# Kernel optimization log

Measured on AMD Instinct MI355X. Metric: run time of the kernel, lower is better.

Reference implementation:

```python
import jax, jax.numpy as jnp
import numpy as np

N_NODES = 50000
N_RAND_EDGES = 800000
N_GRAPHS = 16
F_IN = 128
HID = 64
EMB = 16


def gat_layer(x, src, dst, W, a_src, a_dst, bias, heads, out_ch, concat):
    # x: [N, Fin]; W: [Fin, heads*out_ch]; a_src/a_dst: [heads, out_ch]
    n = x.shape[0]
    h = (x @ W).reshape(n, heads, out_ch)                      # [N, H, C]
    alpha_src = jnp.sum(h * a_src, axis=-1)                    # [N, H]
    alpha_dst = jnp.sum(h * a_dst, axis=-1)                    # [N, H]
    logits = jax.nn.leaky_relu(alpha_src[src] + alpha_dst[dst], 0.2)  # [E, H]
    # segment softmax over incoming edges of each dst node
    m = jax.ops.segment_max(logits, dst, num_segments=n)       # [N, H]
    e = jnp.exp(logits - m[dst])                               # [E, H]
    s = jax.ops.segment_sum(e, dst, num_segments=n)            # [N, H]
    alpha = e / (s[dst] + 1e-16)                               # [E, H]
    msg = h[src] * alpha[:, :, None]                           # [E, H, C]
    out = jax.ops.segment_sum(msg, dst, num_segments=n)        # [N, H, C]
    out = out.reshape(n, heads * out_ch) if concat else out.mean(axis=1)
    return out + bias, alpha


def setup_inputs() -> dict:
    key = jax.random.key(0)
    ks = jax.random.split(key, 20)
    x = jax.random.normal(ks[0], (N_NODES, F_IN), dtype=jnp.float32)
    src = jax.random.randint(ks[1], (N_RAND_EDGES,), 0, N_NODES)
    dst = jax.random.randint(ks[2], (N_RAND_EDGES,), 0, N_NODES)
    loops = jnp.arange(N_NODES)
    edge_index = jnp.stack([jnp.concatenate([src, loops]),
                            jnp.concatenate([dst, loops])]).astype(jnp.int64)
    batch = jnp.sort(jax.random.randint(ks[3], (N_NODES,), 0, N_GRAPHS)).astype(jnp.int64)
    p = lambda k, shp: (jax.random.normal(k, shp, dtype=jnp.float32) * 0.1)
    return {
        "x": x, "edge_index": edge_index, "batch": batch,
        # conv1: 128 -> 64, heads=2, concat -> 128
        "W1": p(ks[4], (F_IN, 2 * HID)), "as1": p(ks[5], (2, HID)), "ad1": p(ks[6], (2, HID)), "b1": p(ks[7], (2 * HID,)),
        # conv2: 128 -> 128, heads=1, mean
        "W2": p(ks[8], (2 * HID, 2 * HID)), "as2": p(ks[9], (1, 2 * HID)), "ad2": p(ks[10], (1, 2 * HID)), "b2": p(ks[11], (2 * HID,)),
        # conv3: 128 -> 16, heads=1, mean
        "W3": p(ks[12], (2 * HID, EMB)), "as3": p(ks[13], (1, EMB)), "ad3": p(ks[14], (1, EMB)), "b3": p(ks[15], (EMB,)),
        # final classifier 16 -> 2
        "Wl": p(ks[16], (EMB, 2)), "bl": p(ks[17], (2,)),
    }


def reference(x, edge_index, batch, W1, as1, ad1, b1, W2, as2, ad2, b2,
              W3, as3, ad3, b3, Wl, bl):
    src, dst = edge_index[0], edge_index[1]
    h1, a1 = gat_layer(x, src, dst, W1, as1, ad1, b1, heads=2, out_ch=HID, concat=True)
    h1 = jax.nn.relu(h1)
    h2, a2 = gat_layer(h1, src, dst, W2, as2, ad2, b2, heads=1, out_ch=2 * HID, concat=False)
    h2 = jax.nn.relu(h2)
    emb, a3 = gat_layer(h2, src, dst, W3, as3, ad3, b3, heads=1, out_ch=EMB, concat=False)
    # global mean pool over graphs (eval mode -> dropout is identity)
    counts = jax.ops.segment_sum(jnp.ones((emb.shape[0],), emb.dtype), batch, num_segments=N_GRAPHS)
    g_emb = jax.ops.segment_sum(emb, batch, num_segments=N_GRAPHS) / jnp.clip(counts, 1.0, None)[:, None]
    out = g_emb @ Wl + bl
    return (out, g_emb, emb, a1, a2, a3)
```

## Files before the change

kernel.cpp:

```cpp
#include <hip/hip_runtime.h>
#include <hip/hip_bf16.h>

#define DEVFN __device__ __forceinline__

using short8 = __attribute__((ext_vector_type(8))) short;
using f32x4  = __attribute__((ext_vector_type(4))) float;

DEVFN float ldf(const void* p, size_t i, bool f32) {
    return f32 ? ((const float*)p)[i]
               : __bfloat162float(((const __hip_bfloat16*)p)[i]);
}
DEVFN int ldidx(const void* p, size_t i, bool i64) {
    return i64 ? (int)((const long long*)p)[i] : ((const int*)p)[i];
}
DEVFN void stf(void* p, size_t i, float v, bool f32) {
    if (f32) ((float*)p)[i] = v;
    else     ((__hip_bfloat16*)p)[i] = __float2bfloat16(v);
}
DEVFN float lky(float v) { return v > 0.f ? v : 0.2f * v; }

DEVFN float bfbits2f(short s) {
    return __uint_as_float(((unsigned)(unsigned short)s) << 16);
}
DEVFN short f2bfbits(float f) {
    unsigned u = __float_as_uint(f);
    return (short)((u + 0x7fffu + ((u >> 16) & 1u)) >> 16);
}

__global__ void detect_k(const void* x, const void* ei, int* flags) {
    if (threadIdx.x == 0 && blockIdx.x == 0) {
        const __hip_bfloat16* xb = (const __hip_bfloat16*)x;
        int bad = 0;
        for (int i = 0; i < 512; ++i) {
            float v = __bfloat162float(xb[i]);
            if (!(v == v) || fabsf(v) > 1.0e6f) bad++;
        }
        flags[0] = (bad > 16) ? 1 : 0;
        const unsigned* w = (const unsigned*)ei;
        int zeros = 0;
        for (int i = 0; i < 64; ++i) if (w[2 * i + 1] == 0u) zeros++;
        flags[1] = (zeros >= 60) ? 1 : 0;
    }
}

__global__ void zero_i32(int* __restrict__ p, int n) {
    int i = blockIdx.x * blockDim.x + threadIdx.x;
    int st = gridDim.x * blockDim.x;
    for (; i < n; i += st) p[i] = 0;
}
__global__ void zero_f32(float* __restrict__ p, long n) {
    long i = (long)blockIdx.x * blockDim.x + threadIdx.x;
    long st = (long)gridDim.x * blockDim.x;
    for (; i < n; i += st) p[i] = 0.f;
}

__global__ void hist_k(const void* __restrict__ ei, int E, int* __restrict__ cnt,
                       const int* __restrict__ flags) {
    const bool i64 = flags[1] != 0;
    int e = blockIdx.x * blockDim.x + threadIdx.x;
    if (e >= E) return;
    atomicAdd(&cnt[ldidx(ei, (size_t)E + e, i64)], 1);
}

__global__ void scan_block_k(const int* __restrict__ cnt, int* __restrict__ incl,
                             int* __restrict__ part, int N) {
    __shared__ int sm[256];
    int tid = threadIdx.x;
    int i = blockIdx.x * 256 + tid;
    int v = (i < N) ? cnt[i] : 0;
    sm[tid] = v;
    __syncthreads();
    for (int o = 1; o < 256; o <<= 1) {
        int t = (tid >= o) ? sm[tid - o] : 0;
        __syncthreads();
        sm[tid] += t;
        __syncthreads();
    }
    if (i < N) incl[i] = sm[tid];
    if (tid == 255) part[blockIdx.x] = sm[255];
}

__global__ void scan_part_k(int* __restrict__ part, int nb) {
    __shared__ int sm[256];
    __shared__ int off;
    int tid = threadIdx.x;
    if (tid == 0) off = 0;
    __syncthreads();
    for (int b = 0; b < nb; b += 256) {
        int i = b + tid;
        int v = (i < nb) ? part[i] : 0;
        sm[tid] = v;
        __syncthreads();
        for (int o = 1; o < 256; o <<= 1) {
            int t = (tid >= o) ? sm[tid - o] : 0;
            __syncthreads();
            sm[tid] += t;
            __syncthreads();
        }
        if (i < nb) part[i] = sm[tid] - v + off;
        __syncthreads();
        if (tid == 255) off += sm[255];
        __syncthreads();
    }
}

__global__ void finalize_scan_k(int* __restrict__ incl_cur, const int* __restrict__ cnt,
                                const int* __restrict__ part, int* __restrict__ rs,
                                int N, int E) {
    int i = blockIdx.x * 256 + threadIdx.x;
    if (i >= N) return;
    int v = incl_cur[i] - cnt[i] + part[blockIdx.x];
    rs[i] = v;
    incl_cur[i] = v;
    if (i == N - 1) rs[N] = E;
}

__global__ void scatter_csr_k(const void* __restrict__ ei, int E, int* __restrict__ cur,
                              int2* __restrict__ csr, const int* __restrict__ flags) {
    const bool i64 = flags[1] != 0;
    int e = blockIdx.x * blockDim.x + threadIdx.x;
    if (e >= E) return;
    int s = ldidx(ei, e, i64);
    int d = ldidx(ei, (size_t)E + e, i64);
    int p = atomicAdd(&cur[d], 1);
    csr[p] = make_int2(s, e);
}

template <int DSRC, int FOUT, int HEADS>
__global__ __launch_bounds__(256) void gemm_alpha_mfma_k(
    const void* __restrict__ xin, const void* __restrict__ Wv,
    const void* __restrict__ asv, const void* __restrict__ adv,
    short* __restrict__ h_bf, float* __restrict__ as_out, float* __restrict__ ad_out,
    int N, const int* __restrict__ flags)
{
    constexpr int FIN = 128;
    constexpr int NCT = FOUT / 16;
    constexpr int CPH = FOUT / HEADS;
    constexpr int CTPH = CPH / 16;
    const bool f32 = flags[0] != 0;

    __shared__ short Wt[FOUT * FIN];

    for (int i = threadIdx.x; i < FIN * FOUT; i += 256) {
        int k = i / FOUT, c = i - (i / FOUT) * FOUT;
        short w;
        if (f32) w = f2bfbits(((const float*)Wv)[i]);
        else     w = ((const short*)Wv)[i];
        *(short*)((char*)Wt + (size_t)c * (FIN * 2) + (((k * 2) ^ ((c & 7) << 4)))) = w;
    }
    __syncthreads();

    const int wv = threadIdx.x >> 6;
    const int lane = threadIdx.x & 63;
    const int m0 = blockIdx.x * 64 + wv * 16;
    if (m0 >= N) return;
    const int lrow = lane & 15;
    const int lk   = lane >> 4;

    short8 afrag[4];
    if (DSRC == 0 && f32) {
        const float* xf = (const float*)xin + (size_t)(m0 + lrow) * FIN + lk * 8;
#pragma unroll
        for (int ks = 0; ks < 4; ++ks) {
            short8 t;
#pragma unroll
            for (int j = 0; j < 8; ++j) t[j] = f2bfbits(xf[ks * 32 + j]);
            afrag[ks] = t;
        }
    } else {
        const short* xb = (const short*)xin + (size_t)(m0 + lrow) * FIN + lk * 8;
#pragma unroll
        for (int ks = 0; ks < 4; ++ks)
            afrag[ks] = *(const short8*)(xb + ks * 32);
    }

    float csA[HEADS][4], cdA[HEADS][4];
#pragma unroll
    for (int hd = 0; hd < HEADS; ++hd)
#pragma unroll
        for (int r = 0; r < 4; ++r) { csA[hd][r] = 0.f; cdA[hd][r] = 0.f; }

#pragma unroll
    for (int ct = 0; ct < NCT; ++ct) {
        const int col = ct * 16 + lrow;
        const int hd = ct / CTPH;
        f32x4 acc = {0.f, 0.f, 0.f, 0.f};
#pragma unroll
        for (int ks = 0; ks < 4; ++ks) {
            const int kbyte = ks * 64 + lk * 16;
            short8 bfrag = *(const short8*)((const char*)Wt +
                               (size_t)col * (FIN * 2) + (kbyte ^ ((col & 7) << 4)));
            acc = __builtin_amdgcn_mfma_f32_16x16x32_bf16(afrag[ks], bfrag, acc, 0, 0, 0);
        }
        const float asc = ldf(asv, col, f32);
        const float adc = ldf(adv, col, f32);
#pragma unroll
        for (int r = 0; r < 4; ++r) {
            h_bf[(size_t)(m0 + lk * 4 + r) * FOUT + col] = f2bfbits(acc[r]);
            csA[hd][r] += acc[r] * asc;
            cdA[hd][r] += acc[r] * adc;
        }
    }

#pragma unroll
    for (int hd = 0; hd < HEADS; ++hd)
#pragma unroll
        for (int r = 0; r < 4; ++r) {
            float cs = csA[hd][r], cd = cdA[hd][r];
            for (int o = 1; o < 16; o <<= 1) {
                cs += __shfl_xor(cs, o);
                cd += __shfl_xor(cd, o);
            }
            csA[hd][r] = cs; cdA[hd][r] = cd;
        }
    if (lrow == 0) {
#pragma unroll
        for (int r = 0; r < 4; ++r) {
            int n = m0 + lk * 4 + r;
#pragma unroll
            for (int hd = 0; hd < HEADS; ++hd) {
                as_out[(size_t)n * HEADS + hd] = csA[hd][r];
                ad_out[(size_t)n * HEADS + hd] = cdA[hd][r];
            }
        }
    }
}

template <int HEADS, bool RELU>
__global__ __launch_bounds__(256) void agg128_k(
    const short* __restrict__ h_bf, const float* __restrict__ as_,
    const float* __restrict__ ad_, const int* __restrict__ rs,
    const int2* __restrict__ csr, const void* __restrict__ bias,
    short* __restrict__ z_bf, void* __restrict__ dout, size_t aoff,
    int N, const int* __restrict__ flags)
{
    __shared__ int   ls_src[4][64];
    __shared__ float ls_a[4][HEADS][64];
    const bool f32 = flags[0] != 0;
    const int wv = threadIdx.x >> 6;
    const int wid = (blockIdx.x * 256 + threadIdx.x) >> 6;
    if (wid >= N) return;
    const int lane = threadIdx.x & 63;
    const int beg = rs[wid], end = rs[wid + 1];
    const int deg = end - beg;
    const int cg = lane & 15;
    const int es = lane >> 4;
    const int h = (HEADS == 2) ? (cg >> 3) : 0;

    const float ad0 = ad_[(size_t)wid * HEADS];
    const float ad1 = (HEADS == 2) ? ad_[(size_t)wid * HEADS + 1] : 0.f;

    float acc[8] = {0.f, 0.f, 0.f, 0.f, 0.f, 0.f, 0.f, 0.f};

    if (deg <= 64) {
        const bool act = lane < deg;
        int2 se = make_int2(0, 0);
        if (act) se = csr[beg + lane];
        float l0 = act ? lky(as_[(size_t)se.x * HEADS] + ad0) : -1e30f;
        float l1 = 0.f;
        if (HEADS == 2) l1 = act ? lky(as_[(size_t)se.x * HEADS + 1] + ad1) : -1e30f;

        float m0 = l0, m1 = l1;
        for (int o = 1; o < 64; o <<= 1) {
            m0 = fmaxf(m0, __shfl_xor(m0, o));
            if (HEADS == 2) m1 = fmaxf(m1, __shfl_xor(m1, o));
        }
        float e0 = act ? expf(l0 - m0) : 0.f;
        float e1 = (HEADS == 2) ? (act ? expf(l1 - m1) : 0.f) : 0.f;
        float s0 = e0, s1 = e1;
        for (int o = 1; o < 64; o <<= 1) {
            s0 += __shfl_xor(s0, o);
            if (HEADS == 2) s1 += __shfl_xor(s1, o);
        }
        if (act) {
            float a0 = e0 * (1.f / (s0 + 1e-16f));
            ls_src[wv][lane] = se.x;
            ls_a[wv][0][lane] = a0;
            stf(dout, aoff + (size_t)se.y * HEADS, a0, f32);
            if (HEADS == 2) {
                float a1 = e1 * (1.f / (s1 + 1e-16f));
                ls_a[wv][1][lane] = a1;
                stf(dout, aoff + (size_t)se.y * 2 + 1, a1, f32);
            }
        }
        for (int b = 0; b < deg; b += 8) {
            const int pA = b + es, pB = b + 4 + es;
            int sA = 0, sB = 0;
            float aA = 0.f, aB = 0.f;
            if (pA < deg) { sA = ls_src[wv][pA]; aA = ls_a[wv][h][pA]; }
            if (pB < deg) { sB = ls_src[wv][pB]; aB = ls_a[wv][h][pB]; }
            const short8 hA = *(const short8*)(h_bf + (size_t)sA * 128 + cg * 8);
            const short8 hB = *(const short8*)(h_bf + (size_t)sB * 128 + cg * 8);
#pragma unroll
            for (int j = 0; j < 8; ++j) acc[j] = fmaf(bfbits2f(hA[j]), aA, acc[j]);
#pragma unroll
            for (int j = 0; j < 8; ++j) acc[j] = fmaf(bfbits2f(hB[j]), aB, acc[j]);
        }
    } else {
        float m0 = -1e30f, m1 = -1e30f;
        for (int p = beg + lane; p < end; p += 64) {
            int s = csr[p].x;
            m0 = fmaxf(m0, lky(as_[(size_t)s * HEADS] + ad0));
            if (HEADS == 2) m1 = fmaxf(m1, lky(as_[(size_t)s * HEADS + 1] + ad1));
        }
        for (int o = 1; o < 64; o <<= 1) {
            m0 = fmaxf(m0, __shfl_xor(m0, o));
            if (HEADS == 2) m1 = fmaxf(m1, __shfl_xor(m1, o));
        }
        float s0 = 0.f, s1 = 0.f;
        for (int p = beg + lane; p < end; p += 64) {
            int s = csr[p].x;
            s0 += expf(lky(as_[(size_t)s * HEADS] + ad0) - m0);
            if (HEADS == 2) s1 += expf(lky(as_[(size_t)s * HEADS + 1] + ad1) - m1);
        }
        for (int o = 1; o < 64; o <<= 1) {
            s0 += __shfl_xor(s0, o);
            if (HEADS == 2) s1 += __shfl_xor(s1, o);
        }
        const float inv0 = 1.f / (s0 + 1e-16f);
        const float inv1 = 1.f / (s1 + 1e-16f);

        for (int cb = beg; cb < end; cb += 64) {
            const int cn = min(64, end - cb);
            if (lane < cn) {
                int2 se = csr[cb + lane];
                float a0 = expf(lky(as_[(size_t)se.x * HEADS] + ad0) - m0) * inv0;
                ls_src[wv][lane] = se.x;
                ls_a[wv][0][lane] = a0;
                stf(dout, aoff + (size_t)se.y * HEADS, a0, f32);
                if (HEADS == 2) {
                    float a1 = expf(lky(as_[(size_t)se.x * HEADS + 1] + ad1) - m1) * inv1;
                    ls_a[wv][1][lane] = a1;
                    stf(dout, aoff + (size_t)se.y * 2 + 1, a1, f32);
                }
            }
            for (int b = 0; b < cn; b += 8) {
                const int pA = b + es, pB = b + 4 + es;
                int sA = 0, sB = 0;
                float aA = 0.f, aB = 0.f;
                if (pA < cn) { sA = ls_src[wv][pA]; aA = ls_a[wv][h][pA]; }
                if (pB < cn) { sB = ls_src[wv][pB]; aB = ls_a[wv][h][pB]; }
                const short8 hA = *(const short8*)(h_bf + (size_t)sA * 128 + cg * 8);
                const short8 hB = *(const short8*)(h_bf + (size_t)sB * 128 + cg * 8);
#pragma unroll
                for (int j = 0; j < 8; ++j) acc[j] = fmaf(bfbits2f(hA[j]), aA, acc[j]);
#pragma unroll
                for (int j = 0; j < 8; ++j) acc[j] = fmaf(bfbits2f(hB[j]), aB, acc[j]);
            }
        }
    }

#pragma unroll
    for (int j = 0; j < 8; ++j) {
        acc[j] += __shfl_xor(acc[j], 16);
        acc[j] += __shfl_xor(acc[j], 32);
    }
    if (es == 0) {
        short8 outv;
#pragma unroll
        for (int j = 0; j < 8; ++j) {
            float v = acc[j] + ldf(bias, cg * 8 + j, f32);
            if (RELU) v = fmaxf(v, 0.f);
            outv[j] = f2bfbits(v);
        }
        *(short8*)(z_bf + (size_t)wid * 128 + cg * 8) = outv;
    }
}

__global__ __launch_bounds__(256) void agg16_k(
    const short* __restrict__ h_bf, const float* __restrict__ as_,
    const float* __restrict__ ad_, const int* __restrict__ rs,
    const int2* __restrict__ csr, float* __restrict__ out,
    void* __restrict__ dout, size_t aoff, int N, const int* __restrict__ flags)
{
    __shared__ int   ls_src[4][64];
    __shared__ float ls_a[4][64];
    const bool f32 = flags[0] != 0;
    const int wv = threadIdx.x >> 6;
    const int wid = (blockIdx.x * 256 + threadIdx.x) >> 6;
    if (wid >= N) return;
    const int lane = threadIdx.x & 63;
    const int beg = rs[wid], end = rs[wid + 1];
    const int deg = end - beg;
    const int cg = lane & 7;
    const int es = lane >> 3;

    const float ad0 = ad_[wid];

    float a0s = 0.f, a1s = 0.f;

    if (deg <= 64) {
        const bool act = lane < deg;
        int2 se = make_int2(0, 0);
        if (act) se = csr[beg + lane];
        float l0 = act ? lky(as_[se.x] + ad0) : -1e30f;
        float m0 = l0;
        for (int o = 1; o < 64; o <<= 1) m0 = fmaxf(m0, __shfl_xor(m0, o));
        float e0 = act ? expf(l0 - m0) : 0.f;
        float s0 = e0;
        for (int o = 1; o < 64; o <<= 1) s0 += __shfl_xor(s0, o);
        if (act) {
            float a0 = e0 * (1.f / (s0 + 1e-16f));
            ls_src[wv][lane] = se.x;
            ls_a[wv][lane] = a0;
            stf(dout, aoff + se.y, a0, f32);
        }
        for (int b = 0; b < deg; b += 8) {
            const int p = b + es;
            if (p < deg) {
                const int sj = ls_src[wv][p];
                const float a = ls_a[wv][p];
                const int hv = *(const int*)(h_bf + (size_t)sj * 16 + cg * 2);
                a0s = fmaf(bfbits2f((short)(hv & 0xffff)), a, a0s);
                a1s = fmaf(bfbits2f((short)(hv >> 16)), a, a1s);
            }
        }
    } else {
        float m0 = -1e30f;
        for (int p = beg + lane; p < end; p += 64)
            m0 = fmaxf(m0, lky(as_[csr[p].x] + ad0));
        for (int o = 1; o < 64; o <<= 1) m0 = fmaxf(m0, __shfl_xor(m0, o));
        float s0 = 0.f;
        for (int p = beg + lane; p < end; p += 64)
            s0 += expf(lky(as_[csr[p].x] + ad0) - m0);
        for (int o = 1; o < 64; o <<= 1) s0 += __shfl_xor(s0, o);
        const float inv0 = 1.f / (s0 + 1e-16f);

        for (int cb = beg; cb < end; cb += 64) {
            const int cn = min(64, end - cb);
            if (lane < cn) {
                int2 se = csr[cb + lane];
                float a0 = expf(lky(as_[se.x] + ad0) - m0) * inv0;
                ls_src[wv][lane] = se.x;
                ls_a[wv][lane] = a0;
                stf(dout, aoff + se.y, a0, f32);
            }
            for (int b = 0; b < cn; b += 8) {
                const int p = b + es;
                if (p < cn) {
                    const int sj = ls_src[wv][p];
                    const float a = ls_a[wv][p];
                    const int hv = *(const int*)(h_bf + (size_t)sj * 16 + cg * 2);
                    a0s = fmaf(bfbits2f((short)(hv & 0xffff)), a, a0s);
                    a1s = fmaf(bfbits2f((short)(hv >> 16)), a, a1s);
                }
            }
        }
    }

#pragma unroll
    for (int o = 8; o < 64; o <<= 1) {
        a0s += __shfl_xor(a0s, o);
        a1s += __shfl_xor(a1s, o);
    }
    if (es == 0) {
        out[(size_t)wid * 16 + cg * 2]     = a0s;
        out[(size_t)wid * 16 + cg * 2 + 1] = a1s;
    }
}

__global__ __launch_bounds__(256) void finalize3_k(
    const float* __restrict__ acc, const void* __restrict__ bias,
    const void* __restrict__ batch, void* __restrict__ dout, size_t emb_off,
    float* __restrict__ g_sum, int N, const int* __restrict__ flags)
{
    const bool f32 = flags[0] != 0;
    const bool i64 = flags[1] != 0;
    __shared__ float gp[256];
    int tid = threadIdx.x;
    gp[tid] = 0.f;
    __syncthreads();
    long idx = (long)blockIdx.x * 256 + tid;
    if (idx < (long)N * 16) {
        int n = (int)(idx >> 4), col = (int)(idx & 15);
        float v = acc[idx] + ldf(bias, col, f32);
        stf(dout, emb_off + idx, v, f32);
        int g = ldidx(batch, n, i64);
        atomicAdd(&gp[g * 16 + col], v);
    }
    __syncthreads();
    float pv = gp[tid];
    if (pv != 0.f) atomicAdd(&g_sum[tid], pv);
}

__global__ __launch_bounds__(256) void head_k(
    const float* __restrict__ g_sum, const void* __restrict__ batch,
    const void* __restrict__ Wl, const void* __restrict__ bl,
    void* __restrict__ dout, size_t gemb_off, int N, const int* __restrict__ flags)
{
    const bool f32 = flags[0] != 0;
    const bool i64 = flags[1] != 0;
    __shared__ float ge[256];
    __shared__ int cnts[16];
    int tid = threadIdx.x;
    if (tid < 16) {
        int lo = 0, hi = N;
        while (lo < hi) { int mid = (lo + hi) >> 1; if (ldidx(batch, mid, i64) < tid) lo = mid + 1; else hi = mid; }
        int l2 = 0, h2 = N;
        while (l2 < h2) { int mid = (l2 + h2) >> 1; if (ldidx(batch, mid, i64) <= tid) l2 = mid + 1; else h2 = mid; }
        cnts[tid] = l2 - lo;
    }
    __syncthreads();
    {
        int g = tid >> 4;
        float v = g_sum[tid] / fmaxf((float)cnts[g], 1.f);
        ge[tid] = v;
        stf(dout, gemb_off + tid, v, f32);
    }
    __syncthreads();
    if (tid < 32) {
        int g = tid >> 1, j = tid & 1;
        float s = ldf(bl, j, f32);
        for (int c = 0; c < 16; ++c) s += ge[g * 16 + c] * ldf(Wl, (size_t)c * 2 + j, f32);
        stf(dout, (size_t)g * 2 + j, s, f32);
    }
}

static inline int cdiv(long a, int b) { return (int)((a + b - 1) / b); }

extern "C" void kernel_launch(void* const* d_in, const int* in_sizes, int n_in,
                              void* d_out, int out_size, void* d_ws, size_t ws_size,
                              hipStream_t stream)
{
    const void* x   = d_in[0];
    const void* ei  = d_in[1];
    const void* batch = d_in[2];
    const void* W1  = d_in[3];
    const void* as1 = d_in[4];
    const void* ad1 = d_in[5];
    const void* b1  = d_in[6];
    const void* W2  = d_in[7];
    const void* as2 = d_in[8];
    const void* ad2 = d_in[9];
    const void* b2  = d_in[10];
    const void* W3  = d_in[11];
    const void* as3 = d_in[12];
    const void* ad3 = d_in[13];
    const void* b3  = d_in[14];
    const void* Wl  = d_in[15];
    const void* bl  = d_in[16];

    const int N = in_sizes[0] / 128;
    const int E = in_sizes[1] / 2;

    int* flags = (int*)d_ws;
    float* ws = (float*)d_ws + 16;
    size_t o = 0;
    float* as_  = ws + o; o += (size_t)N * 2;
    float* ad_  = ws + o; o += (size_t)N * 2;
    float* bufE = ws + o; o += (size_t)N * 16;
    float* g_sum = ws + o; o += 256;
    short* hX = (short*)(ws + o); o += (size_t)N * 64;
    short* hZ = (short*)(ws + o); o += (size_t)N * 64;
    short* h3 = (short*)(ws + o); o += (size_t)N * 8;
    int* ip = (int*)(ws + o);
    int* cnt  = ip;            ip += N;
    int* incl = ip;            ip += N;
    int* part = ip;            ip += 256;
    int* rs   = ip;            ip += N + 1;
    if (((uintptr_t)ip & 7) != 0) ip += 1;
    int2* csr = (int2*)ip;     ip += 2 * E;

    const size_t off_gemb = 32;
    const size_t off_emb  = 32 + 256;
    const size_t off_a1   = off_emb + (size_t)N * 16;
    const size_t off_a2   = off_a1 + (size_t)E * 2;
    const size_t off_a3   = off_a2 + (size_t)E;

    const int B = 256;
    const int nbN = cdiv(N, 256);
    const int gemmBlocks = cdiv(N, 64);
    const int waveBlocks = cdiv(N, 4);

    detect_k<<<1, 64, 0, stream>>>(x, ei, flags);

    zero_i32<<<nbN, B, 0, stream>>>(cnt, N);
    hist_k<<<cdiv(E, B), B, 0, stream>>>(ei, E, cnt, flags);
    scan_block_k<<<nbN, B, 0, stream>>>(cnt, incl, part, N);
    scan_part_k<<<1, B, 0, stream>>>(part, nbN);
    finalize_scan_k<<<nbN, B, 0, stream>>>(incl, cnt, part, rs, N, E);
    scatter_csr_k<<<cdiv(E, B), B, 0, stream>>>(ei, E, incl, csr, flags);

    gemm_alpha_mfma_k<0, 128, 2><<<gemmBlocks, 256, 0, stream>>>(x, W1, as1, ad1, hX, as_, ad_, N, flags);
    agg128_k<2, true><<<waveBlocks, 256, 0, stream>>>(hX, as_, ad_, rs, csr, b1, hZ,
                                                      d_out, off_a1, N, flags);

    gemm_alpha_mfma_k<1, 128, 1><<<gemmBlocks, 256, 0, stream>>>(hZ, W2, as2, ad2, hX, as_, ad_, N, flags);
    agg128_k<1, true><<<waveBlocks, 256, 0, stream>>>(hX, as_, ad_, rs, csr, b2, hZ,
                                                      d_out, off_a2, N, flags);

    gemm_alpha_mfma_k<1, 16, 1><<<gemmBlocks, 256, 0, stream>>>(hZ, W3, as3, ad3, h3, as_, ad_, N, flags);
    agg16_k<<<waveBlocks, 256, 0, stream>>>(h3, as_, ad_, rs, csr, bufE,
                                            d_out, off_a3, N, flags);
    zero_f32<<<1, B, 0, stream>>>(g_sum, 256);
    finalize3_k<<<cdiv((long)N * 16, B), B, 0, stream>>>(bufE, b3, batch, d_out, off_emb, g_sum, N, flags);

    head_k<<<1, B, 0, stream>>>(g_sum, batch, Wl, bl, d_out, off_gemb, N, flags);
}
```

Baseline: 349.8 us.

## Build CSR via two-pass bucketed scatter to localize atomic writes

Replaces the single random CSR scatter with a two-level scatter. Edges are first grouped into buckets of 128 destination nodes using padded per-bucket counters, then each bucket is scattered into the final CSR by one block. The goal is to make the final atomics and writes land in a small, cache-local region instead of being spread randomly over the whole array. The cost is an extra pass that writes and reads a 16-byte-per-edge intermediate buffer, plus heavily contended atomics on about 400 bucket counters.

```diff
diff --git a/kernel.cpp b/kernel.cpp
--- a/kernel.cpp
+++ b/kernel.cpp
@@ -55,11 +55,13 @@
 }
 
 __global__ void hist_k(const void* __restrict__ ei, int E, int* __restrict__ cnt,
-                       const int* __restrict__ flags) {
+                       int* __restrict__ bcnt, const int* __restrict__ flags) {
     const bool i64 = flags[1] != 0;
     int e = blockIdx.x * blockDim.x + threadIdx.x;
     if (e >= E) return;
-    atomicAdd(&cnt[ldidx(ei, (size_t)E + e, i64)], 1);
+    int d = ldidx(ei, (size_t)E + e, i64);
+    atomicAdd(&cnt[d], 1);
+    atomicAdd(&bcnt[(d >> 7) * 16], 1);
 }
 
 __global__ void scan_block_k(const int* __restrict__ cnt, int* __restrict__ incl,
@@ -115,15 +117,53 @@
     if (i == N - 1) rs[N] = E;
 }
 
-__global__ void scatter_csr_k(const void* __restrict__ ei, int E, int* __restrict__ cur,
-                              int2* __restrict__ csr, const int* __restrict__ flags) {
+__global__ void bucket_scan_k(const int* __restrict__ bcnt, int* __restrict__ bbase,
+                              int* __restrict__ bcur, int NB, int E) {
+    __shared__ int sm[256];
+    __shared__ int off;
+    int tid = threadIdx.x;
+    if (tid == 0) off = 0;
+    __syncthreads();
+    for (int b = 0; b < NB; b += 256) {
+        int i = b + tid;
+        int v = (i < NB) ? bcnt[i * 16] : 0;
+        sm[tid] = v;
+        __syncthreads();
+        for (int o = 1; o < 256; o <<= 1) {
+            int t = (tid >= o) ? sm[tid - o] : 0;
+            __syncthreads();
+            sm[tid] += t;
+            __syncthreads();
+        }
+        if (i < NB) { int ex = sm[tid] - v + off; bbase[i] = ex; bcur[i * 16] = ex; }
+        __syncthreads();
+        if (tid == 255) off += sm[255];
+        __syncthreads();
+    }
+    if (tid == 0) bbase[NB] = E;
+}
+
+__global__ void bucket_scatter_k(const void* __restrict__ ei, int E, int* __restrict__ bcur,
+                                 int4* __restrict__ bk, const int* __restrict__ flags) {
     const bool i64 = flags[1] != 0;
     int e = blockIdx.x * blockDim.x + threadIdx.x;
     if (e >= E) return;
     int s = ldidx(ei, e, i64);
     int d = ldidx(ei, (size_t)E + e, i64);
-    int p = atomicAdd(&cur[d], 1);
-    csr[p] = make_int2(s, e);
+    int p = atomicAdd(&bcur[(d >> 7) * 16], 1);
+    bk[p] = make_int4(s, d, e, 0);
+}
+
+__global__ void final_scatter_k(const int4* __restrict__ bk, const int* __restrict__ bbase,
+                                int* __restrict__ cur, int2* __restrict__ csr, int NB) {
+    int b = blockIdx.x;
+    if (b >= NB) return;
+    const int beg = bbase[b], end = bbase[b + 1];
+    for (int i = beg + threadIdx.x; i < end; i += blockDim.x) {
+        int4 v = bk[i];
+        int p = atomicAdd(&cur[v.y], 1);
+        csr[p] = make_int2(v.x, v.z);
+    }
 }
 
 template <int DSRC, int FOUT, int HEADS>
@@ -542,6 +582,7 @@
 
     const int N = in_sizes[0] / 128;
     const int E = in_sizes[1] / 2;
+    const int NB = (N + 127) >> 7;
 
     int* flags = (int*)d_ws;
     float* ws = (float*)d_ws + 16;
@@ -554,12 +595,16 @@
     short* hZ = (short*)(ws + o); o += (size_t)N * 64;
     short* h3 = (short*)(ws + o); o += (size_t)N * 8;
     int* ip = (int*)(ws + o);
-    int* cnt  = ip;            ip += N;
-    int* incl = ip;            ip += N;
-    int* part = ip;            ip += 256;
-    int* rs   = ip;            ip += N + 1;
-    if (((uintptr_t)ip & 7) != 0) ip += 1;
-    int2* csr = (int2*)ip;     ip += 2 * E;
+    int* cnt   = ip;           ip += N;
+    int* bcnt  = ip;           ip += NB * 16;
+    int* incl  = ip;           ip += N;
+    int* part  = ip;           ip += 256;
+    int* rs    = ip;           ip += N + 1;
+    int* bbase = ip;           ip += NB + 1;
+    int* bcur  = ip;           ip += NB * 16;
+    if (((uintptr_t)ip & 15) != 0) ip += 4 - (((uintptr_t)ip >> 2) & 3);
+    int4* bk = (int4*)ip;      ip += 4 * (size_t)E;
+    int2* csr = (int2*)ip;     ip += 2 * (size_t)E;
 
     const size_t off_gemb = 32;
     const size_t off_emb  = 32 + 256;
@@ -574,12 +619,14 @@
 
     detect_k<<<1, 64, 0, stream>>>(x, ei, flags);
 
-    zero_i32<<<nbN, B, 0, stream>>>(cnt, N);
-    hist_k<<<cdiv(E, B), B, 0, stream>>>(ei, E, cnt, flags);
+    zero_i32<<<cdiv(N + NB * 16, B), B, 0, stream>>>(cnt, N + NB * 16);
+    hist_k<<<cdiv(E, B), B, 0, stream>>>(ei, E, cnt, bcnt, flags);
     scan_block_k<<<nbN, B, 0, stream>>>(cnt, incl, part, N);
     scan_part_k<<<1, B, 0, stream>>>(part, nbN);
     finalize_scan_k<<<nbN, B, 0, stream>>>(incl, cnt, part, rs, N, E);
-    scatter_csr_k<<<cdiv(E, B), B, 0, stream>>>(ei, E, incl, csr, flags);
+    bucket_scan_k<<<1, B, 0, stream>>>(bcnt, bbase, bcur, NB, E);
+    bucket_scatter_k<<<cdiv(E, B), B, 0, stream>>>(ei, E, bcur, bk, flags);
+    final_scatter_k<<<NB, B, 0, stream>>>(bk, bbase, incl, csr, NB);
 
     gemm_alpha_mfma_k<0, 128, 2><<<gemmBlocks, 256, 0, stream>>>(x, W1, as1, ad1, hX, as_, ad_, N, flags);
     agg128_k<2, true><<<waveBlocks, 256, 0, stream>>>(hX, as_, ad_, rs, csr, b1, hZ,
```

After: 420.1 us. 20.1% more time.
